# Kernel tuning notes

Measured on AMD Instinct MI355X. Metric: run time of the kernel, lower is better.

The kernel has to match this reference:

```python
import jax, jax.numpy as jnp
import numpy as np

B, T, H, L, V = 256, 20, 512, 2, 8964
LQ, LH, LI = 40, 80, 49
BETA = 3.0


def setup_inputs() -> dict:
    key = jax.random.key(0)
    ks = iter(jax.random.split(key, 40))
    s = 1.0 / np.sqrt(H)
    n = lambda shape, sc=s: jax.random.normal(next(ks), shape, jnp.float32) * sc
    inp = {
        'emb': n((B, T, H), 1.0),
        'question': n((B, LQ, 2 * H), 1.0),
        'history': n((B, LH, 2 * H), 1.0),
        'image': n((B, LI, 2 * H), 1.0),
        'h0': jnp.zeros((L, B, H), jnp.float32),
        'c0': jnp.zeros((L, B, H), jnp.float32),
        # LSTM params (both layers have input dim H since ninp == nhid)
        'Wih': n((L, 4 * H, H)), 'Whh': n((L, 4 * H, H)),
        'bih': jnp.zeros((L, 4 * H), jnp.float32), 'bhh': jnp.zeros((L, 4 * H), jnp.float32),
        # question attention: w_q (2H->H), ans_q (H->H), Wa_q (H->1)
        'Wq': n((H, 2 * H)), 'bq': jnp.zeros((H,), jnp.float32),
        'Wansq': n((H, H)), 'bansq': jnp.zeros((H,), jnp.float32),
        'waq': n((1, H)), 'baq': jnp.zeros((1,), jnp.float32),
        # history attention
        'Wh': n((H, 2 * H)), 'bh': jnp.zeros((H,), jnp.float32),
        'Wansh': n((H, H)), 'bansh': jnp.zeros((H,), jnp.float32),
        'wah': n((1, H)), 'bah': jnp.zeros((1,), jnp.float32),
        # image attention
        'Wi': n((H, 2 * H)), 'bi': jnp.zeros((H,), jnp.float32),
        'Wansi': n((H, H)), 'bansi': jnp.zeros((H,), jnp.float32),
        'wai': n((1, H)), 'bai': jnp.zeros((1,), jnp.float32),
        # concat fusion (3H -> H)
        'Wcat': n((H, 3 * H)), 'bcat': jnp.zeros((H,), jnp.float32),
        # decoder SimpleClassifier: 2H -> 4H -> V
        'Wd1': n((4 * H, 2 * H)), 'bd1': jnp.zeros((4 * H,), jnp.float32),
        'Wd2': n((V, 4 * H), 1.0 / np.sqrt(4 * H)), 'bd2': jnp.zeros((V,), jnp.float32),
    }
    return inp


def reference(emb, question, history, image, h0, c0,
              Wih, Whh, bih, bhh,
              Wq, bq, Wansq, bansq, waq, baq,
              Wh, bh, Wansh, bansh, wah, bah,
              Wi, bi, Wansi, bansi, wai, bai,
              Wcat, bcat, Wd1, bd1, Wd2, bd2):
    nlayers = Wih.shape[0]
    # context projections are timestep-invariant: hoist out of the loop
    q_emb = question @ Wq.T + bq   # [B, LQ, H]
    h_emb = history @ Wh.T + bh    # [B, LH, H]
    i_emb = image @ Wi.T + bi      # [B, LI, H]

    def attend(ctx, out, Wans, bans, wa, ba):
        # ctx: [B, Lx, H], out: [B, H]
        a = jnp.tanh(ctx + (out @ Wans.T + bans)[:, None, :])
        logits = jnp.einsum('blh,h->bl', a, wa[0]) + ba[0]
        w = jax.nn.softmax(logits, axis=1)
        return jnp.einsum('bl,blh->bh', w, ctx)

    def step(carry, x_t):
        h, c = carry  # each [L, B, H]
        inp = x_t
        hs, cs = [], []
        for l in range(nlayers):
            gates = inp @ Wih[l].T + h[l] @ Whh[l].T + bih[l] + bhh[l]
            gi, gf, gg, go = jnp.split(gates, 4, axis=-1)  # torch gate order i,f,g,o
            cn = jax.nn.sigmoid(gf) * c[l] + jax.nn.sigmoid(gi) * jnp.tanh(gg)
            hn = jax.nn.sigmoid(go) * jnp.tanh(cn)
            hs.append(hn); cs.append(cn)
            inp = hn
        out = inp  # top-layer output [B, H]
        fq = attend(q_emb, out, Wansq, bansq, waq, baq)
        fh = attend(h_emb, out, Wansh, bansh, wah, bah)
        fi = attend(i_emb, out, Wansi, bansi, wai, bai)
        cat = jnp.tanh(jnp.concatenate([fq, fh, fi], axis=1) @ Wcat.T + bcat)
        fusion = jnp.concatenate([out, cat], axis=1)  # [B, 2H]
        dec = jax.nn.relu(fusion @ Wd1.T + bd1) @ Wd2.T + bd2
        lp = jax.nn.log_softmax(BETA * dec, axis=1)
        return (jnp.stack(hs), jnp.stack(cs)), lp

    (hT, cT), lps = jax.lax.scan(step, (h0, c0), jnp.swapaxes(emb, 0, 1))
    return jnp.swapaxes(lps, 0, 1), hT, cT
```

## Files before the change

### kernel.cpp

```cpp
#include <hip/hip_runtime.h>
#include <cmath>

#define B_ 256
#define T_ 20
#define H_ 512
#define V_ 8964
#define LQ_ 40
#define LH_ 80
#define LI_ 49
#define BT_ (B_ * T_)
#define BH_ (B_ * H_)
#define NPAD_ 9088
#define BETA_ 3.0f

typedef __attribute__((ext_vector_type(8))) short bf16x8;
typedef __attribute__((ext_vector_type(4))) float f32x4;
typedef __attribute__((ext_vector_type(8))) unsigned short u16x8;

static __device__ __forceinline__ unsigned short f2bf(float f) {
    union { float f; unsigned u; } v; v.f = f;
    unsigned r = v.u + 0x7FFF + ((v.u >> 16) & 1);
    return (unsigned short)(r >> 16);
}
static __device__ __forceinline__ float bf2f(unsigned short u) {
    union { unsigned u; float f; } v; v.u = ((unsigned)u) << 16;
    return v.f;
}
static __device__ __forceinline__ float fast_tanh(float x) {
    const float e = __expf(2.f * x);
    return 1.f - 2.f * __builtin_amdgcn_rcpf(e + 1.f);
}
static __device__ __forceinline__ float fast_sigmoid(float x) {
    return __builtin_amdgcn_rcpf(1.f + __expf(-x));
}
static __device__ __forceinline__ void st16_sc(unsigned short* p, unsigned short v) {
    unsigned int vv = v;
    asm volatile("global_store_short %0, %1, off sc0 sc1" :: "v"(p), "v"(vv) : "memory");
}
#define GLD16(g, l) __builtin_amdgcn_global_load_lds(                                   \
    (const __attribute__((address_space(1))) unsigned int*)(unsigned long long)(const void*)(g), \
    (__attribute__((address_space(3))) unsigned int*)(unsigned int)(unsigned long long)(void*)(l), \
    16, 0, 0)

__global__ __launch_bounds__(256) void cvt_kernel(
    const float* __restrict__ src, unsigned short* __restrict__ dst,
    long long srcRows, long long cols, long long dstRows)
{
    const long long total = dstRows * cols;
    const long long e0 = ((long long)blockIdx.x * 256 + threadIdx.x) * 8;
    if (e0 >= total) return;
    const long long row = e0 / cols;
    u16x8 v;
    if (row < srcRows) {
        float4 a = *reinterpret_cast<const float4*>(src + e0);
        float4 b = *reinterpret_cast<const float4*>(src + e0 + 4);
        v[0] = f2bf(a.x); v[1] = f2bf(a.y); v[2] = f2bf(a.z); v[3] = f2bf(a.w);
        v[4] = f2bf(b.x); v[5] = f2bf(b.y); v[6] = f2bf(b.z); v[7] = f2bf(b.w);
    } else {
        v = (u16x8)0;
    }
    *reinterpret_cast<u16x8*>(dst + e0) = v;
}

static void cvt(hipStream_t s, const float* src, unsigned short* dst,
                long long srcRows, long long cols, long long dstRows)
{
    long long total = dstRows * cols;
    cvt_kernel<<<dim3((unsigned)((total / 8 + 255) / 256)), dim3(256), 0, s>>>(
        src, dst, srcRows, cols, dstRows);
}

struct WcvtArgs { const float* src[8]; unsigned short* dst[8]; };

__global__ __launch_bounds__(256) void wcvt_kernel(WcvtArgs a)
{
    static constexpr long long SZ[8] = {524288, 524288, 524288, 262144,
                                        262144, 262144, 786432, 2097152};
    long long off = (long long)blockIdx.x * 2048;
    int seg = 0;
#pragma unroll
    for (int i = 0; i < 8; ++i)
        if (seg == i && off >= SZ[i]) { off -= SZ[i]; ++seg; }
    const float* src = a.src[seg];
    unsigned short* dst = a.dst[seg];
    const long long e = off + (long long)threadIdx.x * 8;
    float4 x = *reinterpret_cast<const float4*>(src + e);
    float4 y = *reinterpret_cast<const float4*>(src + e + 4);
    u16x8 v;
    v[0] = f2bf(x.x); v[1] = f2bf(x.y); v[2] = f2bf(x.z); v[3] = f2bf(x.w);
    v[4] = f2bf(y.x); v[5] = f2bf(y.y); v[6] = f2bf(y.z); v[7] = f2bf(y.w);
    *reinterpret_cast<u16x8*>(dst + e) = v;
}

__global__ __launch_bounds__(256) void cvt_perm_kernel(
    const float* __restrict__ src, unsigned short* __restrict__ dst)
{
    const long long e0 = ((long long)blockIdx.x * 256 + threadIdx.x) * 8;
    if (e0 >= 2048LL * 512) return;
    const int drow = (int)(e0 >> 9);
    const int col = (int)(e0 & 511);
    const int g = (drow >> 4) & 3;
    const int hsrc = ((drow >> 6) << 4) | (drow & 15);
    const int srow = (g << 9) | hsrc;
    const float* sp = src + (long long)srow * 512 + col;
    float4 a = *reinterpret_cast<const float4*>(sp);
    float4 b = *reinterpret_cast<const float4*>(sp + 4);
    u16x8 v;
    v[0] = f2bf(a.x); v[1] = f2bf(a.y); v[2] = f2bf(a.z); v[3] = f2bf(a.w);
    v[4] = f2bf(b.x); v[5] = f2bf(b.y); v[6] = f2bf(b.z); v[7] = f2bf(b.w);
    *reinterpret_cast<u16x8*>(dst + e0) = v;
}

__global__ __launch_bounds__(256) void bias_perm_kernel(
    const float* __restrict__ b1, const float* __restrict__ b2,
    float* __restrict__ dst)
{
    const int n = blockIdx.x * 256 + threadIdx.x;
    if (n < 2048) {
        const int g = (n >> 4) & 3;
        const int h = ((n >> 6) << 4) | (n & 15);
        const int orig = (g << 9) | h;
        dst[n] = b1[orig] + b2[orig];
    }
}

static __device__ __forceinline__ int4 ldA8f(const float* A, long long idx)
{
    const float* p = A + idx;
    float4 a = *reinterpret_cast<const float4*>(p);
    float4 b = *reinterpret_cast<const float4*>(p + 4);
    union { int4 i4; unsigned short u[8]; } r;
    r.u[0] = f2bf(a.x); r.u[1] = f2bf(a.y); r.u[2] = f2bf(a.z); r.u[3] = f2bf(a.w);
    r.u[4] = f2bf(b.x); r.u[5] = f2bf(b.y); r.u[6] = f2bf(b.z); r.u[7] = f2bf(b.w);
    return r.i4;
}

template <int ACT, int OUTBF, int AF32>
__global__ __launch_bounds__(256, 2) void mfma_gemm(
    const void* __restrict__ A, const unsigned short* __restrict__ W,
    const float* __restrict__ bias1, const float* __restrict__ bias2,
    void* __restrict__ C, long long ldc, int Nreal, int K)
{
    __shared__ __align__(16) unsigned short As[2][128][32];
    __shared__ __align__(16) unsigned short Bs[2][128][32];
    const int tid = threadIdx.x;
    const int lane = tid & 63;
    const int wave = tid >> 6;
    const int wm = wave >> 1, wn = wave & 1;

    const int nwg = gridDim.x * gridDim.y;
    const int orig = blockIdx.y * gridDim.x + blockIdx.x;
    const int xcd = orig & 7, base = orig >> 3;
    const int q8 = nwg >> 3, r8 = nwg & 7;
    const int wg = (xcd < r8 ? xcd * (q8 + 1) : r8 * (q8 + 1) + (xcd - r8) * q8) + base;

    int MI = 8192 / (K << AF32);
    if (MI < 1) MI = 1;
    if (MI > (int)gridDim.y) MI = gridDim.y;
    const int slabSz = gridDim.x * MI;
    const int fullSlabs = gridDim.y / MI;
    const int fullRegion = fullSlabs * slabSz;
    int m0, n0;
    if (wg < fullRegion) {
        const int mb = wg / slabSz, rem = wg % slabSz;
        m0 = (mb * MI + rem % MI) * 128;
        n0 = (rem / MI) * 128;
    } else {
        const int rem = wg - fullRegion;
        const int TM = gridDim.y - fullSlabs * MI;
        m0 = (fullSlabs * MI + rem % TM) * 128;
        n0 = (rem / TM) * 128;
    }

    const int r = tid >> 2;
    const int ck = (tid & 3) * 8;

    const unsigned short* Wp = W + (long long)n0 * K;

    f32x4 acc[4][4] = {};
    int cur = 0;

    if constexpr (!AF32) {
        const unsigned short* Ab = (const unsigned short*)A;
        auto issue = [&](int k0, int buf) {
            const unsigned short* ga0 = Ab + (long long)(m0 + r) * K + k0 + ck;
            const unsigned short* ga1 = Ab + (long long)(m0 + r + 64) * K + k0 + ck;
            const unsigned short* gb0 = Wp + (long long)r * K + k0 + ck;
            const unsigned short* gb1 = Wp + (long long)(r + 64) * K + k0 + ck;
            char* lA = (char*)&As[buf][0][0] + wave * 1024;
            char* lB = (char*)&Bs[buf][0][0] + wave * 1024;
            GLD16(ga0, lA);
            GLD16(ga1, lA + 4096);
            GLD16(gb0, lB);
            GLD16(gb1, lB + 4096);
        };
        issue(0, 0);
        for (int k0 = 0; k0 < K; k0 += 32, cur ^= 1) {
            __syncthreads();
            if (k0 + 32 < K) issue(k0 + 32, cur ^ 1);
            const int lr = lane & 15, lk = (lane >> 4) * 8;
            bf16x8 af[4], bfr[4];
#pragma unroll
            for (int i = 0; i < 4; ++i) {
                af[i]  = *reinterpret_cast<const bf16x8*>(&As[cur][wm * 64 + i * 16 + lr][lk]);
                bfr[i] = *reinterpret_cast<const bf16x8*>(&Bs[cur][wn * 64 + i * 16 + lr][lk]);
            }
#pragma unroll
            for (int i = 0; i < 4; ++i)
#pragma unroll
                for (int j = 0; j < 4; ++j)
                    acc[i][j] = __builtin_amdgcn_mfma_f32_16x16x32_bf16(
                        af[i], bfr[j], acc[i][j], 0, 0, 0);
        }
    } else {
        const float* Af = (const float*)A;
        int4 ra0, ra1, rb0, rb1;
        ra0 = ldA8f(Af, (long long)(m0 + r) * K + ck);
        ra1 = ldA8f(Af, (long long)(m0 + r + 64) * K + ck);
        rb0 = *reinterpret_cast<const int4*>(Wp + (long long)r * K + ck);
        rb1 = *reinterpret_cast<const int4*>(Wp + (long long)(r + 64) * K + ck);
        for (int k0 = 0; k0 < K; k0 += 32, cur ^= 1) {
            *reinterpret_cast<int4*>(&As[cur][r][ck]) = ra0;
            *reinterpret_cast<int4*>(&As[cur][r + 64][ck]) = ra1;
            *reinterpret_cast<int4*>(&Bs[cur][r][ck]) = rb0;
            *reinterpret_cast<int4*>(&Bs[cur][r + 64][ck]) = rb1;
            __syncthreads();
            if (k0 + 32 < K) {
                const int kn = k0 + 32 + ck;
                ra0 = ldA8f(Af, (long long)(m0 + r) * K + kn);
                ra1 = ldA8f(Af, (long long)(m0 + r + 64) * K + kn);
                rb0 = *reinterpret_cast<const int4*>(Wp + (long long)r * K + kn);
                rb1 = *reinterpret_cast<const int4*>(Wp + (long long)(r + 64) * K + kn);
            }
            const int lr = lane & 15, lk = (lane >> 4) * 8;
            bf16x8 af[4], bfr[4];
#pragma unroll
            for (int i = 0; i < 4; ++i) {
                af[i]  = *reinterpret_cast<const bf16x8*>(&As[cur][wm * 64 + i * 16 + lr][lk]);
                bfr[i] = *reinterpret_cast<const bf16x8*>(&Bs[cur][wn * 64 + i * 16 + lr][lk]);
            }
#pragma unroll
            for (int i = 0; i < 4; ++i)
#pragma unroll
                for (int j = 0; j < 4; ++j)
                    acc[i][j] = __builtin_amdgcn_mfma_f32_16x16x32_bf16(
                        af[i], bfr[j], acc[i][j], 0, 0, 0);
        }
    }

    const int lr = lane & 15, lrow4 = (lane >> 4) * 4;
#pragma unroll
    for (int j = 0; j < 4; ++j) {
        const int col = n0 + wn * 64 + j * 16 + lr;
        if (col >= Nreal) continue;
        float bsum = 0.f;
        if (bias1) bsum += bias1[col];
        if (bias2) bsum += bias2[col];
#pragma unroll
        for (int i = 0; i < 4; ++i) {
#pragma unroll
            for (int rr = 0; rr < 4; ++rr) {
                const int row = m0 + wm * 64 + i * 16 + lrow4 + rr;
                float v = acc[i][j][rr] + bsum;
                if (ACT == 1) v = fast_tanh(v);
                if (ACT == 2) v = fmaxf(v, 0.f);
                if (OUTBF)
                    ((unsigned short*)C)[(long long)row * ldc + col] = f2bf(v);
                else
                    ((float*)C)[(long long)row * ldc + col] = v;
            }
        }
    }
}

static void mgemm(hipStream_t s, int act, int outbf, int af32,
                  const void* A, const unsigned short* W,
                  const float* b1, const float* b2,
                  void* C, long long ldc, int M, int Nreal, int K)
{
    dim3 grid((Nreal + 127) / 128, M / 128), blk(256);
#define MG(a, o, f) mfma_gemm<a, o, f><<<grid, blk, 0, s>>>(A, W, b1, b2, C, ldc, Nreal, K)
    if (af32) {
        if (outbf) { if (act == 1) MG(1,1,1); else if (act == 2) MG(2,1,1); else MG(0,1,1); }
        else       { if (act == 1) MG(1,0,1); else if (act == 2) MG(2,0,1); else MG(0,0,1); }
    } else {
        if (outbf) { if (act == 1) MG(1,1,0); else if (act == 2) MG(2,1,0); else MG(0,1,0); }
        else       { if (act == 1) MG(1,0,0); else if (act == 2) MG(2,0,0); else MG(0,0,0); }
    }
#undef MG
}

#define LSTM_ISSUE(b_, dst_) do {                                              \
    const unsigned short* pa_ = (((b_) >> 2) ? q20 : q10) + ((b_) & 3) * 128;  \
    const unsigned short* pb_ = (((b_) >> 2) ? q21 : q11) + ((b_) & 3) * 128;  \
    asm volatile(                                                              \
        "global_load_dwordx4 %0, %[pa], off sc0 sc1\n\t"                       \
        "global_load_dwordx4 %1, %[pa], off offset:64 sc0 sc1\n\t"             \
        "global_load_dwordx4 %2, %[pa], off offset:128 sc0 sc1\n\t"            \
        "global_load_dwordx4 %3, %[pa], off offset:192 sc0 sc1\n\t"            \
        "global_load_dwordx4 %4, %[pb], off sc0 sc1\n\t"                       \
        "global_load_dwordx4 %5, %[pb], off offset:64 sc0 sc1\n\t"             \
        "global_load_dwordx4 %6, %[pb], off offset:128 sc0 sc1\n\t"            \
        "global_load_dwordx4 %7, %[pb], off offset:192 sc0 sc1"                \
        : "=&v"((dst_)[0]), "=&v"((dst_)[1]), "=&v"((dst_)[2]), "=&v"((dst_)[3]), \
          "=&v"((dst_)[4]), "=&v"((dst_)[5]), "=&v"((dst_)[6]), "=&v"((dst_)[7])  \
        : [pa] "v"(pa_), [pb] "v"(pb_)                                         \
        : "memory");                                                           \
} while (0)

__global__ __launch_bounds__(256, 1) void lstm_persistent_kernel(
    const unsigned short* __restrict__ emb_bf,
    const unsigned short* __restrict__ Wih0p, const unsigned short* __restrict__ Whh0p,
    const unsigned short* __restrict__ Wih1p, const unsigned short* __restrict__ Whh1p,
    const float* __restrict__ bp0, const float* __restrict__ bp1,
    const float* __restrict__ c0,
    unsigned short* __restrict__ hbuf,
    float* __restrict__ st_h, float* __restrict__ st_c,
    unsigned short* __restrict__ h_top,
    int* flags)
{
    __shared__ __align__(16) unsigned short Wlds[2][64][512];

    const int gid = blockIdx.x;
    const int grp = gid >> 6;
    const int id  = gid & 63;
    const int mt = id >> 5, nt = id & 31;
    const int m0 = mt * 128, n0 = nt * 64;
    const int tid = threadIdx.x;
    const int lane = tid & 63;
    const int w = tid >> 6;
    const int lr = lane & 15;
    const int hi = lane >> 4;
    const int hi4 = hi * 4;

    const unsigned short* W1g = (grp ? Wih1p : Wih0p) + (long long)n0 * H_;
    const unsigned short* W2g = (grp ? Whh1p : Whh0p) + (long long)n0 * H_;

#pragma unroll
    for (int it = 0; it < 16; ++it) {
        const int e = (tid + it * 256) * 8;
        const int row = e >> 9, col = e & 511;
        const int bir = (col * 2) ^ ((row & 7) << 4);
        char* dst = (char*)Wlds + row * 1024 + bir;
        *reinterpret_cast<int4*>(dst) =
            *reinterpret_cast<const int4*>(W1g + (long long)row * H_ + col);
        *reinterpret_cast<int4*>(dst + 65536) =
            *reinterpret_cast<const int4*>(W2g + (long long)row * H_ + col);
    }
    __syncthreads();

    const int h = nt * 16 + lr;
    const float* bp = grp ? bp1 : bp0;
    float bg[4];
#pragma unroll
    for (int g = 0; g < 4; ++g) bg[g] = bp[n0 + g * 16 + lr];

    const int ar0 = m0 + w * 32 + lr;
    const int ar1 = ar0 + 16;

    float cregA[4], cregB[4], hn0[4], hn1[4];
#pragma unroll
    for (int rr = 0; rr < 4; ++rr) {
        cregA[rr] = c0[(long long)grp * BH_ + (long long)(m0 + w * 32 + hi4 + rr) * H_ + h];
        cregB[rr] = c0[(long long)grp * BH_ + (long long)(m0 + w * 32 + 16 + hi4 + rr) * H_ + h];
    }

    int bbase[4];
#pragma unroll
    for (int j = 0; j < 4; ++j)
        bbase[j] = (j * 16 + lr) * 1024 + ((hi * 16) ^ ((lr & 3) << 4));
    const int xk6 = ((lr >> 2) & 1) << 6;

    int* myFlag = flags + (mt * 64 + grp * 32 + nt) * 16;
    const long long sEmb = (long long)T_ * H_;

    for (int s = 0; s <= T_; ++s) {
        const bool active = (grp == 0) ? (s < T_) : (s >= 1);
        const int t = grp ? (s - 1) : s;
        if (active) {
            const unsigned short *A1, *A2;
            long long sA1;
            unsigned short* hout;
            if (grp == 0) {
                A1 = emb_bf + (long long)t * H_; sA1 = sEmb;
                A2 = hbuf + (long long)(s % 3) * BH_;
                hout = hbuf + (long long)((s + 1) % 3) * BH_;
            } else {
                A1 = hbuf + (long long)(s % 3) * BH_; sA1 = H_;
                A2 = hbuf + (long long)(3 + (s & 1)) * BH_;
                hout = hbuf + (long long)(3 + ((s + 1) & 1)) * BH_;
            }
            const unsigned short* q10 = A1 + (long long)ar0 * sA1 + hi * 8;
            const unsigned short* q11 = A1 + (long long)ar1 * sA1 + hi * 8;
            const unsigned short* q20 = A2 + (long long)ar0 * H_ + hi * 8;
            const unsigned short* q21 = A2 + (long long)ar1 * H_ + hi * 8;

            int4 buf[3][8];
            LSTM_ISSUE(0, buf[0]);
            LSTM_ISSUE(1, buf[1]);
            LSTM_ISSUE(2, buf[2]);

            f32x4 accA[4] = {}, accB[4] = {};
#pragma unroll
            for (int b = 0; b < 8; ++b) {
                if (b < 6)      asm volatile("s_waitcnt vmcnt(16)" ::: "memory");
                else if (b == 6) asm volatile("s_waitcnt vmcnt(8)" ::: "memory");
                else             asm volatile("s_waitcnt vmcnt(0)" ::: "memory");
                __builtin_amdgcn_sched_barrier(0);
#pragma unroll
                for (int i = 0; i < 4; ++i) {
                    const int it = b * 4 + i;
                    const int kk = it & 15, p = it >> 4;
                    const bf16x8 a0 = *reinterpret_cast<const bf16x8*>(&buf[b % 3][i]);
                    const bf16x8 a1 = *reinterpret_cast<const bf16x8*>(&buf[b % 3][4 + i]);
                    const int kb = ((kk << 6) ^ xk6) + (p << 16);
#pragma unroll
                    for (int j = 0; j < 4; ++j) {
                        const bf16x8 bfv = *reinterpret_cast<const bf16x8*>(
                            (const char*)Wlds + bbase[j] + kb);
                        accA[j] = __builtin_amdgcn_mfma_f32_16x16x32_bf16(a0, bfv, accA[j], 0, 0, 0);
                        accB[j] = __builtin_amdgcn_mfma_f32_16x16x32_bf16(a1, bfv, accB[j], 0, 0, 0);
                    }
                }
                if (b + 3 < 8) LSTM_ISSUE(b + 3, buf[b % 3]);
            }

#pragma unroll
            for (int rr = 0; rr < 4; ++rr) {
                {
                    const int b = m0 + w * 32 + hi4 + rr;
                    const float i_ = fast_sigmoid(accA[0][rr] + bg[0]);
                    const float f_ = fast_sigmoid(accA[1][rr] + bg[1]);
                    const float g_ = fast_tanh(accA[2][rr] + bg[2]);
                    const float o_ = fast_sigmoid(accA[3][rr] + bg[3]);
                    const float cn = f_ * cregA[rr] + i_ * g_;
                    const float hn = o_ * fast_tanh(cn);
                    cregA[rr] = cn; hn0[rr] = hn;
                    st16_sc(&hout[(long long)b * H_ + h], f2bf(hn));
                }
                {
                    const int b = m0 + w * 32 + 16 + hi4 + rr;
                    const float i_ = fast_sigmoid(accB[0][rr] + bg[0]);
                    const float f_ = fast_sigmoid(accB[1][rr] + bg[1]);
                    const float g_ = fast_tanh(accB[2][rr] + bg[2]);
                    const float o_ = fast_sigmoid(accB[3][rr] + bg[3]);
                    const float cn = f_ * cregB[rr] + i_ * g_;
                    const float hn = o_ * fast_tanh(cn);
                    cregB[rr] = cn; hn1[rr] = hn;
                    st16_sc(&hout[(long long)b * H_ + h], f2bf(hn));
                }
            }
            if (s == T_) {
#pragma unroll
                for (int rr = 0; rr < 4; ++rr) {
                    const int b0r = m0 + w * 32 + hi4 + rr;
                    const int b1r = b0r + 16;
                    h_top[((long long)b0r * T_ + t) * H_ + h] = f2bf(hn0[rr]);
                    h_top[((long long)b1r * T_ + t) * H_ + h] = f2bf(hn1[rr]);
                    st_h[(long long)grp * BH_ + (long long)b0r * H_ + h] = hn0[rr];
                    st_h[(long long)grp * BH_ + (long long)b1r * H_ + h] = hn1[rr];
                    st_c[(long long)grp * BH_ + (long long)b0r * H_ + h] = cregA[rr];
                    st_c[(long long)grp * BH_ + (long long)b1r * H_ + h] = cregB[rr];
                }
            }
        }
        if (s < T_) {
            __syncthreads();
            if (tid == 0) {
                int v = s + 1;
                asm volatile("global_store_dword %0, %1, off sc0 sc1"
                             :: "v"(myFlag), "v"(v) : "memory");
            }
            if (active) {
#pragma unroll
                for (int rr = 0; rr < 4; ++rr) {
                    const int b0r = m0 + w * 32 + hi4 + rr;
                    const int b1r = b0r + 16;
                    if (grp == 1) {
                        h_top[((long long)b0r * T_ + t) * H_ + h] = f2bf(hn0[rr]);
                        h_top[((long long)b1r * T_ + t) * H_ + h] = f2bf(hn1[rr]);
                    }
                    if (t == T_ - 1) {
                        st_h[(long long)grp * BH_ + (long long)b0r * H_ + h] = hn0[rr];
                        st_h[(long long)grp * BH_ + (long long)b1r * H_ + h] = hn1[rr];
                        st_c[(long long)grp * BH_ + (long long)b0r * H_ + h] = cregA[rr];
                        st_c[(long long)grp * BH_ + (long long)b1r * H_ + h] = cregB[rr];
                    }
                }
            }
            if (tid < 64) {
                const int thr = (grp == 0 && tid >= 32) ? s : s + 1;
                volatile const int* fp = flags + (mt * 64 + tid) * 16;
                while (*fp < thr) __builtin_amdgcn_s_sleep(2);
            }
            __syncthreads();
        }
    }
}

__global__ __launch_bounds__(256) void attend3_kernel(
    const unsigned short* __restrict__ q_emb, const unsigned short* __restrict__ h_emb,
    const unsigned short* __restrict__ i_emb,
    const float* __restrict__ proj3,
    const float* __restrict__ waq, const float* __restrict__ baq, const float* __restrict__ bansq,
    const float* __restrict__ wah, const float* __restrict__ bah, const float* __restrict__ bansh,
    const float* __restrict__ wai, const float* __restrict__ bai, const float* __restrict__ bansi,
    const unsigned short* __restrict__ h_top,
    unsigned short* __restrict__ fcat, unsigned short* __restrict__ fusion)
{
    __shared__ float p_lds[512];
    __shared__ float wa_lds[512];
    __shared__ float lg[96];
    const int bt0 = blockIdx.x;
    const int bt = (bt0 & 7) * (BT_ / 8) + (bt0 >> 3);
    const int c = blockIdx.y;
    const int b = bt / T_;
    const int tid = threadIdx.x;
    const int wid = tid >> 6, lane = tid & 63;

    if (c == 0 && tid < 64)
        *reinterpret_cast<u16x8*>(&fusion[(long long)bt * 1024 + tid * 8]) =
            *reinterpret_cast<const u16x8*>(&h_top[(long long)bt * 512 + tid * 8]);

    const unsigned short* ctx = c == 0 ? q_emb : c == 1 ? h_emb : i_emb;
    const int Lx = c == 0 ? LQ_ : c == 1 ? LH_ : LI_;
    const float* wa = c == 0 ? waq : c == 1 ? wah : wai;
    const float bav = (c == 0 ? baq : c == 1 ? bah : bai)[0];
    const float* bans = c == 0 ? bansq : c == 1 ? bansh : bansi;

    p_lds[tid]       = proj3[(long long)bt * 1536 + c * 512 + tid] + bans[tid];
    p_lds[tid + 256] = proj3[(long long)bt * 1536 + c * 512 + tid + 256] + bans[tid + 256];
    wa_lds[tid] = wa[tid];
    wa_lds[tid + 256] = wa[tid + 256];
    __syncthreads();

    for (int l = wid; l < Lx; l += 4) {
        const unsigned short* crow = ctx + ((long long)b * Lx + l) * H_;
        float acc = 0.f;
#pragma unroll
        for (int j = 0; j < 8; ++j) {
            const int hp = lane + 64 * j;
            acc += wa_lds[hp] * fast_tanh(bf2f(crow[hp]) + p_lds[hp]);
        }
        for (int o = 32; o > 0; o >>= 1) acc += __shfl_down(acc, o);
        if (lane == 0) lg[l] = acc + bav;
    }
    __syncthreads();
    if (tid == 0) {
        float m = -1e30f;
        for (int l = 0; l < Lx; ++l) m = fmaxf(m, lg[l]);
        float ssum = 0.f;
        for (int l = 0; l < Lx; ++l) { const float e = __expf(lg[l] - m); lg[l] = e; ssum += e; }
        const float inv = __builtin_amdgcn_rcpf(ssum);
        for (int l = 0; l < Lx; ++l) lg[l] *= inv;
    }
    __syncthreads();
    for (int hp = tid; hp < H_; hp += 256) {
        float acc = 0.f;
        for (int l = 0; l < Lx; ++l)
            acc += lg[l] * bf2f(ctx[((long long)b * Lx + l) * H_ + hp]);
        fcat[(long long)bt * 1536 + c * 512 + hp] = f2bf(acc);
    }
}

__global__ __launch_bounds__(256) void log_softmax_kernel(float* __restrict__ out)
{
    __shared__ float red[4];
    __shared__ float bc;
    const long long base = (long long)blockIdx.x * V_;
    const int tid = threadIdx.x, lane = tid & 63, wid = tid >> 6;

    float r[36];
    float m = -1e30f;
#pragma unroll
    for (int i = 0; i < 36; ++i) {
        const int v = tid + i * 256;
        r[i] = (v < V_) ? BETA_ * out[base + v] : -1e30f;
        m = fmaxf(m, r[i]);
    }
    for (int o = 32; o > 0; o >>= 1) m = fmaxf(m, __shfl_down(m, o));
    if (lane == 0) red[wid] = m;
    __syncthreads();
    if (tid == 0)
        bc = fmaxf(fmaxf(red[0], red[1]), fmaxf(red[2], red[3]));
    __syncthreads();
    m = bc;

    float s = 0.f;
#pragma unroll
    for (int i = 0; i < 36; ++i) s += __expf(r[i] - m);
    for (int o = 32; o > 0; o >>= 1) s += __shfl_down(s, o);
    if (lane == 0) red[wid] = s;
    __syncthreads();
    if (tid == 0) bc = m + logf(red[0] + red[1] + red[2] + red[3]);
    __syncthreads();
    const float ls = bc;
#pragma unroll
    for (int i = 0; i < 36; ++i) {
        const int v = tid + i * 256;
        if (v < V_) out[base + v] = r[i] - ls;
    }
}

extern "C" void kernel_launch(void* const* d_in, const int* in_sizes, int n_in,
                              void* d_out_, int out_size, void* d_ws, size_t ws_size,
                              hipStream_t stream)
{
    const float* emb      = (const float*)d_in[0];
    const float* question = (const float*)d_in[1];
    const float* history  = (const float*)d_in[2];
    const float* image    = (const float*)d_in[3];
    const float* h0       = (const float*)d_in[4];
    const float* c0       = (const float*)d_in[5];
    const float* Wih      = (const float*)d_in[6];
    const float* Whh      = (const float*)d_in[7];
    const float* bih      = (const float*)d_in[8];
    const float* bhh      = (const float*)d_in[9];
    const float* Wq    = (const float*)d_in[10]; const float* bq    = (const float*)d_in[11];
    const float* Wansq = (const float*)d_in[12]; const float* bansq = (const float*)d_in[13];
    const float* waq   = (const float*)d_in[14]; const float* baq   = (const float*)d_in[15];
    const float* Wh    = (const float*)d_in[16]; const float* bh    = (const float*)d_in[17];
    const float* Wansh = (const float*)d_in[18]; const float* bansh = (const float*)d_in[19];
    const float* wah   = (const float*)d_in[20]; const float* bah   = (const float*)d_in[21];
    const float* Wi    = (const float*)d_in[22]; const float* bi    = (const float*)d_in[23];
    const float* Wansi = (const float*)d_in[24]; const float* bansi = (const float*)d_in[25];
    const float* wai   = (const float*)d_in[26]; const float* bai   = (const float*)d_in[27];
    const float* Wcat  = (const float*)d_in[28]; const float* bcat  = (const float*)d_in[29];
    const float* Wd1   = (const float*)d_in[30]; const float* bd1   = (const float*)d_in[31];
    const float* Wd2   = (const float*)d_in[32]; const float* bd2   = (const float*)d_in[33];

    float* out = (float*)d_out_;

    int*   flags = (int*)d_ws;
    float* st_h = (float*)((char*)d_ws + 8192);
    float* st_c = st_h + 2LL * BH_;
    float* bp0  = st_c + 2LL * BH_;
    float* bp1  = bp0 + 2048;
    unsigned short* hbuf   = (unsigned short*)(bp1 + 2048);
    unsigned short* Wih0p  = hbuf + 5LL * BH_;
    unsigned short* Whh0p  = Wih0p + 2048LL * H_;
    unsigned short* Wih1p  = Whh0p + 2048LL * H_;
    unsigned short* Whh1p  = Wih1p + 2048LL * H_;
    unsigned short* emb_bf = Whh1p + 2048LL * H_;
    unsigned short* h_top_bf = emb_bf + (long long)BT_ * H_;
    unsigned short* q_emb_bf = h_top_bf + (long long)BT_ * H_;
    unsigned short* h_emb_bf = q_emb_bf + (long long)B_ * LQ_ * H_;
    unsigned short* i_emb_bf = h_emb_bf + (long long)B_ * LH_ * H_;
    unsigned short* dec1_bf  = i_emb_bf + (long long)B_ * LI_ * H_;
    unsigned short* Wd2p_bf  = dec1_bf + (long long)BT_ * 4 * H_;

    unsigned short* Wq_bf    = (unsigned short*)out;
    unsigned short* Wh_bf    = Wq_bf + 524288;
    unsigned short* Wi_bf    = Wh_bf + 524288;
    unsigned short* Wansq_bf = Wi_bf + 524288;
    unsigned short* Wansh_bf = Wansq_bf + 262144;
    unsigned short* Wansi_bf = Wansh_bf + 262144;
    unsigned short* Wcat_bf  = Wansi_bf + 262144;
    unsigned short* Wd1_bf   = Wcat_bf + 786432;
    float* proj3 = (float*)(Wd1_bf + 2097152);
    unsigned short* fcat_bf   = (unsigned short*)(proj3 + (long long)BT_ * 1536);
    unsigned short* fusion_bf = fcat_bf + (long long)BT_ * 1536;

    {
        WcvtArgs a;
        a.src[0] = Wq;    a.dst[0] = Wq_bf;
        a.src[1] = Wh;    a.dst[1] = Wh_bf;
        a.src[2] = Wi;    a.dst[2] = Wi_bf;
        a.src[3] = Wansq; a.dst[3] = Wansq_bf;
        a.src[4] = Wansh; a.dst[4] = Wansh_bf;
        a.src[5] = Wansi; a.dst[5] = Wansi_bf;
        a.src[6] = Wcat;  a.dst[6] = Wcat_bf;
        a.src[7] = Wd1;   a.dst[7] = Wd1_bf;
        wcvt_kernel<<<dim3(2560), dim3(256), 0, stream>>>(a);
    }
    cvt(stream, Wd2, Wd2p_bf, V_, (long long)4 * H_, NPAD_);

    cvt(stream, emb, emb_bf, 1, (long long)BT_ * H_, 1);
    cvt_perm_kernel<<<dim3(512), dim3(256), 0, stream>>>(Wih, Wih0p);
    cvt_perm_kernel<<<dim3(512), dim3(256), 0, stream>>>(Whh, Whh0p);
    cvt_perm_kernel<<<dim3(512), dim3(256), 0, stream>>>(Wih + 2048LL * H_, Wih1p);
    cvt_perm_kernel<<<dim3(512), dim3(256), 0, stream>>>(Whh + 2048LL * H_, Whh1p);
    bias_perm_kernel<<<dim3(8), dim3(256), 0, stream>>>(bih, bhh, bp0);
    bias_perm_kernel<<<dim3(8), dim3(256), 0, stream>>>(bih + 2048, bhh + 2048, bp1);
    cvt(stream, h0, hbuf, 1, BH_, 1);
    cvt(stream, h0 + BH_, hbuf + 4LL * BH_, 1, BH_, 1);
    hipMemsetAsync(flags, 0, 8192, stream);

    mgemm(stream, 0, 1, 1, question, Wq_bf, bq, nullptr, q_emb_bf, H_, B_ * LQ_, H_, 2 * H_);
    mgemm(stream, 0, 1, 1, history,  Wh_bf, bh, nullptr, h_emb_bf, H_, B_ * LH_, H_, 2 * H_);
    mgemm(stream, 0, 1, 1, image,    Wi_bf, bi, nullptr, i_emb_bf, H_, B_ * LI_, H_, 2 * H_);

    lstm_persistent_kernel<<<dim3(128), dim3(256), 0, stream>>>(
        emb_bf, Wih0p, Whh0p, Wih1p, Whh1p, bp0, bp1, c0,
        hbuf, st_h, st_c, h_top_bf, flags);

    mgemm(stream, 0, 0, 0, h_top_bf, Wansq_bf, nullptr, nullptr, proj3, 1536, BT_, 1536, H_);
    attend3_kernel<<<dim3(BT_, 3), dim3(256), 0, stream>>>(
        q_emb_bf, h_emb_bf, i_emb_bf, proj3,
        waq, baq, bansq, wah, bah, bansh, wai, bai, bansi,
        h_top_bf, fcat_bf, fusion_bf);

    mgemm(stream, 1, 1, 0, fcat_bf, Wcat_bf, bcat, nullptr, fusion_bf + H_, 2 * H_, BT_, H_, 3 * H_);

    mgemm(stream, 2, 1, 0, fusion_bf, Wd1_bf, bd1, nullptr, dec1_bf, 4 * H_, BT_, 4 * H_, 2 * H_);
    mgemm(stream, 0, 0, 0, dec1_bf, Wd2p_bf, bd2, nullptr, out, V_, BT_, V_, 4 * H_);

    log_softmax_kernel<<<dim3(BT_), dim3(256), 0, stream>>>(out);

    hipMemcpyAsync(out + (long long)BT_ * V_, st_h,
                   4LL * BH_ * sizeof(float), hipMemcpyDeviceToDevice, stream);
}
```

Before: 988.0 us.

## Merge context projections and Wd2 conversion into persistent LSTM launch

Builds one combined grid in which the first 128 blocks run the persistent LSTM recurrence, the next blocks compute the question, history and image context projections with an inline bf16 MFMA GEMM, and the remaining blocks convert Wd2 to padded bf16. The goal is to overlap these independent workloads with the latency-bound LSTM, which leaves most CUs idle, and to remove several kernel launches. The risk is that the LSTM blocks spin on cross-block flags and may not all be resident or scheduled early if other blocks fill the CUs first. Every block also now reserves 128KB of LDS, which limits how many can be co-resident.

```diff
diff --git a/kernel.cpp b/kernel.cpp
--- a/kernel.cpp
+++ b/kernel.cpp
@@ -12,6 +12,14 @@
 #define BH_ (B_ * H_)
 #define NPAD_ 9088
 #define BETA_ 3.0f
+
+#define MEGA_LSTM_ 128
+#define MEGA_CTXQ_ 320
+#define MEGA_CTXH_ 640
+#define MEGA_CTXI_ 392
+#define MEGA_CTX_ (MEGA_CTXQ_ + MEGA_CTXH_ + MEGA_CTXI_)
+#define MEGA_CVT_ 2272
+#define MEGA_GRID_ (MEGA_LSTM_ + MEGA_CTX_ + MEGA_CVT_)
 
 typedef __attribute__((ext_vector_type(8))) short bf16x8;
 typedef __attribute__((ext_vector_type(4))) float f32x4;
@@ -308,7 +316,7 @@
         : "memory");                                                           \
 } while (0)
 
-__global__ __launch_bounds__(256, 1) void lstm_persistent_kernel(
+__global__ __launch_bounds__(256, 1) void mega_kernel(
     const unsigned short* __restrict__ emb_bf,
     const unsigned short* __restrict__ Wih0p, const unsigned short* __restrict__ Whh0p,
     const unsigned short* __restrict__ Wih1p, const unsigned short* __restrict__ Whh1p,
@@ -317,16 +325,115 @@
     unsigned short* __restrict__ hbuf,
     float* __restrict__ st_h, float* __restrict__ st_c,
     unsigned short* __restrict__ h_top,
-    int* flags)
-{
-    __shared__ __align__(16) unsigned short Wlds[2][64][512];
-
+    int* flags,
+    const float* __restrict__ question, const float* __restrict__ history,
+    const float* __restrict__ image,
+    const unsigned short* __restrict__ Wq_bf, const unsigned short* __restrict__ Wh_bf,
+    const unsigned short* __restrict__ Wi_bf,
+    const float* __restrict__ bq, const float* __restrict__ bhb,
+    const float* __restrict__ bi,
+    unsigned short* __restrict__ q_emb, unsigned short* __restrict__ h_emb,
+    unsigned short* __restrict__ i_emb,
+    const float* __restrict__ Wd2, unsigned short* __restrict__ Wd2p)
+{
+    __shared__ __align__(16) char smem[131072];
     const int gid = blockIdx.x;
+    const int tid = threadIdx.x;
+
+    if (gid >= MEGA_LSTM_ + MEGA_CTX_) {
+        const int g = gid - (MEGA_LSTM_ + MEGA_CTX_);
+#pragma unroll
+        for (int i = 0; i < 4; ++i) {
+            const long long e = (long long)g * 8192 + i * 2048 + tid * 8;
+            const long long row = e >> 11;
+            u16x8 v;
+            if (row < V_) {
+                float4 a = *reinterpret_cast<const float4*>(Wd2 + e);
+                float4 b = *reinterpret_cast<const float4*>(Wd2 + e + 4);
+                v[0] = f2bf(a.x); v[1] = f2bf(a.y); v[2] = f2bf(a.z); v[3] = f2bf(a.w);
+                v[4] = f2bf(b.x); v[5] = f2bf(b.y); v[6] = f2bf(b.z); v[7] = f2bf(b.w);
+            } else {
+                v = (u16x8)0;
+            }
+            *reinterpret_cast<u16x8*>(Wd2p + e) = v;
+        }
+        return;
+    }
+
+    if (gid >= MEGA_LSTM_) {
+        int g = gid - MEGA_LSTM_;
+        const float* A; const unsigned short* W; const float* bias;
+        unsigned short* Cc;
+        if (g < MEGA_CTXQ_)       { A = question; W = Wq_bf; bias = bq;  Cc = q_emb; }
+        else if (g < MEGA_CTXQ_ + MEGA_CTXH_) {
+            g -= MEGA_CTXQ_;        A = history;  W = Wh_bf; bias = bhb; Cc = h_emb; }
+        else { g -= MEGA_CTXQ_ + MEGA_CTXH_; A = image; W = Wi_bf; bias = bi; Cc = i_emb; }
+        const int m0 = (g >> 2) * 128, n0 = (g & 3) * 128;
+        const int K = 1024;
+
+        unsigned short (*As)[128][32] = (unsigned short (*)[128][32])smem;
+        unsigned short (*Bs)[128][32] = (unsigned short (*)[128][32])(smem + 16384);
+        const int lane = tid & 63;
+        const int wave = tid >> 6;
+        const int wm = wave >> 1, wn = wave & 1;
+        const int r = tid >> 2;
+        const int ck = (tid & 3) * 8;
+        const unsigned short* Wp = W + (long long)n0 * K;
+
+        f32x4 acc[4][4] = {};
+        int4 ra0, ra1, rb0, rb1;
+        ra0 = ldA8f(A, (long long)(m0 + r) * K + ck);
+        ra1 = ldA8f(A, (long long)(m0 + r + 64) * K + ck);
+        rb0 = *reinterpret_cast<const int4*>(Wp + (long long)r * K + ck);
+        rb1 = *reinterpret_cast<const int4*>(Wp + (long long)(r + 64) * K + ck);
+        int cur = 0;
+        for (int k0 = 0; k0 < K; k0 += 32, cur ^= 1) {
+            *reinterpret_cast<int4*>(&As[cur][r][ck]) = ra0;
+            *reinterpret_cast<int4*>(&As[cur][r + 64][ck]) = ra1;
+            *reinterpret_cast<int4*>(&Bs[cur][r][ck]) = rb0;
+            *reinterpret_cast<int4*>(&Bs[cur][r + 64][ck]) = rb1;
+            __syncthreads();
+            if (k0 + 32 < K) {
+                const int kn = k0 + 32 + ck;
+                ra0 = ldA8f(A, (long long)(m0 + r) * K + kn);
+                ra1 = ldA8f(A, (long long)(m0 + r + 64) * K + kn);
+                rb0 = *reinterpret_cast<const int4*>(Wp + (long long)r * K + kn);
+                rb1 = *reinterpret_cast<const int4*>(Wp + (long long)(r + 64) * K + kn);
+            }
+            const int lr = lane & 15, lk = (lane >> 4) * 8;
+            bf16x8 af[4], bfr[4];
+#pragma unroll
+            for (int i = 0; i < 4; ++i) {
+                af[i]  = *reinterpret_cast<const bf16x8*>(&As[cur][wm * 64 + i * 16 + lr][lk]);
+                bfr[i] = *reinterpret_cast<const bf16x8*>(&Bs[cur][wn * 64 + i * 16 + lr][lk]);
+            }
+#pragma unroll
+            for (int i = 0; i < 4; ++i)
+#pragma unroll
+                for (int j = 0; j < 4; ++j)
+                    acc[i][j] = __builtin_amdgcn_mfma_f32_16x16x32_bf16(
+                        af[i], bfr[j], acc[i][j], 0, 0, 0);
+        }
+        const int lr = lane & 15, lrow4 = (lane >> 4) * 4;
+#pragma unroll
+        for (int j = 0; j < 4; ++j) {
+            const int col = n0 + wn * 64 + j * 16 + lr;
+            const float bsum = bias[col];
+#pragma unroll
+            for (int i = 0; i < 4; ++i)
+#pragma unroll
+                for (int rr = 0; rr < 4; ++rr) {
+                    const int row = m0 + wm * 64 + i * 16 + lrow4 + rr;
+                    Cc[(long long)row * 512 + col] = f2bf(acc[i][j][rr] + bsum);
+                }
+        }
+        return;
+    }
+
     const int grp = gid >> 6;
     const int id  = gid & 63;
     const int mt = id >> 5, nt = id & 31;
     const int m0 = mt * 128, n0 = nt * 64;
-    const int tid = threadIdx.x;
     const int lane = tid & 63;
     const int w = tid >> 6;
     const int lr = lane & 15;
@@ -341,7 +448,7 @@
         const int e = (tid + it * 256) * 8;
         const int row = e >> 9, col = e & 511;
         const int bir = (col * 2) ^ ((row & 7) << 4);
-        char* dst = (char*)Wlds + row * 1024 + bir;
+        char* dst = smem + row * 1024 + bir;
         *reinterpret_cast<int4*>(dst) =
             *reinterpret_cast<const int4*>(W1g + (long long)row * H_ + col);
         *reinterpret_cast<int4*>(dst + 65536) =
@@ -417,7 +524,7 @@
 #pragma unroll
                     for (int j = 0; j < 4; ++j) {
                         const bf16x8 bfv = *reinterpret_cast<const bf16x8*>(
-                            (const char*)Wlds + bbase[j] + kb);
+                            smem + bbase[j] + kb);
                         accA[j] = __builtin_amdgcn_mfma_f32_16x16x32_bf16(a0, bfv, accA[j], 0, 0, 0);
                         accB[j] = __builtin_amdgcn_mfma_f32_16x16x32_bf16(a1, bfv, accB[j], 0, 0, 0);
                     }
@@ -673,7 +780,6 @@
         a.src[7] = Wd1;   a.dst[7] = Wd1_bf;
         wcvt_kernel<<<dim3(2560), dim3(256), 0, stream>>>(a);
     }
-    cvt(stream, Wd2, Wd2p_bf, V_, (long long)4 * H_, NPAD_);
 
     cvt(stream, emb, emb_bf, 1, (long long)BT_ * H_, 1);
     cvt_perm_kernel<<<dim3(512), dim3(256), 0, stream>>>(Wih, Wih0p);
@@ -686,13 +792,12 @@
     cvt(stream, h0 + BH_, hbuf + 4LL * BH_, 1, BH_, 1);
     hipMemsetAsync(flags, 0, 8192, stream);
 
-    mgemm(stream, 0, 1, 1, question, Wq_bf, bq, nullptr, q_emb_bf, H_, B_ * LQ_, H_, 2 * H_);
-    mgemm(stream, 0, 1, 1, history,  Wh_bf, bh, nullptr, h_emb_bf, H_, B_ * LH_, H_, 2 * H_);
-    mgemm(stream, 0, 1, 1, image,    Wi_bf, bi, nullptr, i_emb_bf, H_, B_ * LI_, H_, 2 * H_);
-
-    lstm_persistent_kernel<<<dim3(128), dim3(256), 0, stream>>>(
+    mega_kernel<<<dim3(MEGA_GRID_), dim3(256), 0, stream>>>(
         emb_bf, Wih0p, Whh0p, Wih1p, Whh1p, bp0, bp1, c0,
-        hbuf, st_h, st_c, h_top_bf, flags);
+        hbuf, st_h, st_c, h_top_bf, flags,
+        question, history, image, Wq_bf, Wh_bf, Wi_bf, bq, bh, bi,
+        q_emb_bf, h_emb_bf, i_emb_bf,
+        Wd2, Wd2p_bf);
 
     mgemm(stream, 0, 0, 0, h_top_bf, Wansq_bf, nullptr, nullptr, proj3, 1536, BT_, 1536, H_);
     attend3_kernel<<<dim3(BT_, 3), dim3(256), 0, stream>>>(
```

After: 937.1 us. 1.05x faster.
